# Performance work log

Measured on AMD Instinct MI355X. Metric: run time of the kernel, lower is better.

The kernel has to match this reference:

```python
import jax, jax.numpy as jnp
import numpy as np

NUM_HEADS = 16


def setup_inputs() -> dict:
    key = jax.random.key(0)
    k0, k1, k2, k3 = jax.random.split(key, 4)
    B, N, C = 8, 1024, 1024
    D = C // NUM_HEADS
    x = jax.random.normal(k0, (B, N, C), dtype=jnp.float32)
    # RoPE angle table [1, N, 1, head_dim]
    rope_freqs = jax.random.uniform(k1, (1, N, 1, D), dtype=jnp.float32) * (2.0 * jnp.pi)
    # qkv: Linear(dim, 3*dim, bias=False); proj: Linear(dim, dim) with bias
    qkv_w = jax.random.normal(k2, (3 * C, C), dtype=jnp.float32) * 0.02
    proj_w = jax.random.normal(k3, (C, C), dtype=jnp.float32) * 0.02
    proj_b = jnp.zeros((C,), dtype=jnp.float32)
    return {"x": x, "rope_freqs": rope_freqs, "qkv_w": qkv_w, "proj_w": proj_w, "proj_b": proj_b}


def _rotate_half(t):
    t1, t2 = jnp.split(t, 2, axis=-1)
    return jnp.concatenate([-t2, t1], axis=-1)


def reference(x, rope_freqs, qkv_w, proj_w, proj_b):
    B, N, C = x.shape
    H = NUM_HEADS
    D = C // H
    scale = D ** (-0.5)
    # QKV projection -> [3, B, H, N, D]
    qkv = (x @ qkv_w.T).reshape(B, N, 3, H, D).transpose(2, 0, 3, 1, 4)
    q, k, v = qkv[0], qkv[1], qkv[2]
    # RoPE: freqs [1, N, 1, D] -> [1, 1, N, D], applied to all tokens (n_special = 0)
    freqs = jnp.transpose(rope_freqs, (0, 2, 1, 3))
    cos = jnp.cos(freqs).astype(q.dtype)
    sin = jnp.sin(freqs).astype(q.dtype)
    q = q * cos + _rotate_half(q) * sin
    k = k * cos + _rotate_half(k) * sin
    # Full materialized attention (as in source)
    attn = jax.nn.softmax(jnp.einsum("bhnd,bhmd->bhnm", q, k) * scale, axis=-1)
    out = jnp.einsum("bhnm,bhmd->bhnd", attn, v)  # [B, H, N, D]
    out = out.transpose(0, 2, 1, 3).reshape(B, N, C)
    return out @ proj_w.T + proj_b
```

## Files before the change

### kernel.cpp

```cpp
#include <hip/hip_runtime.h>


typedef __attribute__((ext_vector_type(8))) short bf16x8;
typedef __attribute__((ext_vector_type(4))) float floatx4;
typedef __attribute__((ext_vector_type(4))) unsigned int u32x4;
typedef __attribute__((ext_vector_type(2))) unsigned int u32x2;

__device__ __forceinline__ void gld16(const void* g, void* l) {
  __builtin_amdgcn_global_load_lds((const __attribute__((address_space(1))) void*)g,
                                   (__attribute__((address_space(3))) void*)l, 16, 0, 0);
}

__device__ __forceinline__ short f2bf(float f) {
  unsigned u = __builtin_bit_cast(unsigned, f);
  u = (u + 0x7FFFu + ((u >> 16) & 1u)) >> 16;
  return (short)u;
}
__device__ __forceinline__ unsigned cvtpk(float lo, float hi) {
  unsigned r;
  asm("v_cvt_pk_bf16_f32 %0, %1, %2" : "=v"(r) : "v"(lo), "v"(hi));
  return r;
}
__device__ __forceinline__ float pexp(float x) {
  float r;
  asm("v_exp_f32 %0, %1" : "=v"(r) : "v"(x));
  return r;
}

__global__ __launch_bounds__(256) void prep_all(const float* __restrict__ sx,
                                                const float* __restrict__ sq,
                                                const float* __restrict__ sp,
                                                short* __restrict__ dst,
                                                const float* __restrict__ ropef,
                                                float2* __restrict__ tbl) {
  int bid = blockIdx.x;
  if (bid < 2048) {
    for (int i = bid * 256 + threadIdx.x; i < 3145728; i += 2048 * 256) {
      const float4* src;
      if (i < 2097152)      src = reinterpret_cast<const float4*>(sx) + i;
      else if (i < 2883584) src = reinterpret_cast<const float4*>(sq) + (i - 2097152);
      else                  src = reinterpret_cast<const float4*>(sp) + (i - 2883584);
      float4 v = *src;
      uint2 o;
      o.x = cvtpk(v.x, v.y);
      o.y = cvtpk(v.z, v.w);
      reinterpret_cast<uint2*>(dst)[i] = o;
    }
  } else {
    int i = (bid - 2048) * 256 + threadIdx.x;
    float v = ropef[i];
    tbl[i] = make_float2(cosf(v), sinf(v));
  }
}

#define QSCALE 0.18033688011112042f

__device__ __forceinline__ void gemm_main(const short* __restrict__ A,
                                          const short* __restrict__ Bm,
                                          short* As, short* Bs,
                                          floatx4 (&acc)[2][4],
                                          int bx, int by) {
  const int tid = threadIdx.x;
  const int wid = tid >> 6, lane = tid & 63;
  const int g = lane >> 4, l15 = lane & 15;
  const int wr = wid >> 2, wc = wid & 3;
  const size_t trow = (size_t)by * 128, tcol = (size_t)bx * 256;
  floatx4 zero = {0.f, 0.f, 0.f, 0.f};
  #pragma unroll
  for (int i = 0; i < 2; ++i)
    #pragma unroll
    for (int j = 0; j < 4; ++j) acc[i][j] = zero;

  auto stage = [&](int buf, int k0) {
    {
      const int cb = wid * 64;
      const int c  = cb + lane;
      const int r  = c >> 3, s = c & 7;
      const int koff = k0 + ((s ^ (r & 7)) << 3);
      gld16(A + (trow + r) * 1024 + koff, As + buf * 8192 + (size_t)cb * 8);
    }
    #pragma unroll
    for (int i = 0; i < 2; ++i) {
      const int cb = (i * 16 + wid) * 64;
      const int c  = cb + lane;
      const int r  = c >> 3, s = c & 7;
      const int koff = k0 + ((s ^ (r & 7)) << 3);
      gld16(Bm + (tcol + r) * 1024 + koff, Bs + buf * 16384 + (size_t)cb * 8);
    }
  };

  stage(0, 0);
  __syncthreads();

  for (int t = 0; t < 16; ++t) {
    const int buf = t & 1;
    if (t < 15) stage(buf ^ 1, (t + 1) * 64);
    const short* Ab = As + buf * 8192;
    const short* Bb = Bs + buf * 16384;
    #pragma unroll
    for (int ks = 0; ks < 2; ++ks) {
      bf16x8 af[2], bfr[4];
      #pragma unroll
      for (int mi = 0; mi < 2; ++mi) {
        int row = wr * 32 + mi * 16 + l15;
        int ch  = (ks * 4 + g) ^ (row & 7);
        af[mi] = *reinterpret_cast<const bf16x8*>(Ab + row * 64 + ch * 8);
      }
      #pragma unroll
      for (int nt = 0; nt < 4; ++nt) {
        int row = wc * 64 + nt * 16 + l15;
        int ch  = (ks * 4 + g) ^ (row & 7);
        bfr[nt] = *reinterpret_cast<const bf16x8*>(Bb + row * 64 + ch * 8);
      }
      __builtin_amdgcn_s_setprio(1);
      #pragma unroll
      for (int mi = 0; mi < 2; ++mi)
        #pragma unroll
        for (int nt = 0; nt < 4; ++nt)
          acc[mi][nt] = __builtin_amdgcn_mfma_f32_16x16x32_bf16(af[mi], bfr[nt],
                                                                acc[mi][nt], 0, 0, 0);
      __builtin_amdgcn_s_setprio(0);
    }
    __syncthreads();
  }
}

__global__ __launch_bounds__(1024, 4) void gemm_qkv_k(const short* __restrict__ A,
                                                      const short* __restrict__ Bm,
                                                      const float2* __restrict__ tbl,
                                                      short* __restrict__ qo,
                                                      short* __restrict__ ko,
                                                      short* __restrict__ vt) {
  extern __shared__ __align__(16) short smem[];
  short* As = smem;
  short* Bs = smem + 16384;
  const int id  = blockIdx.y * 12 + blockIdx.x;
  const int sid = (id & 7) * 96 + (id >> 3);
  const int bx  = sid % 12, by = sid / 12;
  floatx4 acc[2][4];
  gemm_main(A, Bm, As, Bs, acc, bx, by);

  const int tid = threadIdx.x;
  const int wid = tid >> 6, lane = tid & 63;
  const int g = lane >> 4, l15 = lane & 15;
  const int wr = wid >> 2, wc = wid & 3;
  const int trow = by * 128, tcol = bx * 256;
  const int which = bx >> 2;

  if (which < 2) {
    short* dst = which == 0 ? qo : ko;
    const float sc = which == 0 ? QSCALE : 1.0f;
    #pragma unroll
    for (int nt = 0; nt < 2; ++nt) {
      int col = tcol + wc * 64 + nt * 16 + l15;
      int hc = col & 1023, h = hc >> 6, d1 = hc & 63;
      #pragma unroll
      for (int mi = 0; mi < 2; ++mi)
        #pragma unroll
        for (int r = 0; r < 4; ++r) {
          int rowg = trow + wr * 32 + mi * 16 + g * 4 + r;
          int b = rowg >> 10, n = rowg & 1023;
          float a1 = acc[mi][nt][r], a2 = acc[mi][nt + 2][r];
          float2 c1 = tbl[n * 64 + d1];
          float2 c2 = tbl[n * 64 + d1 + 32];
          float o1 = (a1 * c1.x - a2 * c1.y) * sc;
          float o2 = (a2 * c2.x + a1 * c2.y) * sc;
          size_t base = ((size_t)(b * 16 + h) * 1024 + n) * 64;
          dst[base + d1]      = f2bf(o1);
          dst[base + d1 + 32] = f2bf(o2);
        }
    }
  } else {
    #pragma unroll
    for (int nt = 0; nt < 4; ++nt) {
      int col = tcol + wc * 64 + nt * 16 + l15;
      int hc = col & 1023, h = hc >> 6, d = hc & 63;
      #pragma unroll
      for (int mi = 0; mi < 2; ++mi) {
        int rowg = trow + wr * 32 + mi * 16 + g * 4;
        int b = rowg >> 10, n0 = rowg & 1023;
        ushort4 pk;
        pk.x = (unsigned short)f2bf(acc[mi][nt][0]);
        pk.y = (unsigned short)f2bf(acc[mi][nt][1]);
        pk.z = (unsigned short)f2bf(acc[mi][nt][2]);
        pk.w = (unsigned short)f2bf(acc[mi][nt][3]);
        *reinterpret_cast<ushort4*>((unsigned short*)vt +
            ((size_t)(b * 16 + h) * 64 + d) * 1024 + n0) = pk;
      }
    }
  }
}

__global__ __launch_bounds__(1024, 4) void gemm_proj_k(const short* __restrict__ A,
                                                       const short* __restrict__ Bm,
                                                       const float* __restrict__ pb,
                                                       float* __restrict__ out) {
  extern __shared__ __align__(16) short smem[];
  short* As = smem;
  short* Bs = smem + 16384;
  const int id  = blockIdx.y * 4 + blockIdx.x;
  const int sid = (id & 7) * 32 + (id >> 3);
  const int bx  = sid % 4, by = sid / 4;
  floatx4 acc[2][4];
  gemm_main(A, Bm, As, Bs, acc, bx, by);

  const int tid = threadIdx.x;
  const int wid = tid >> 6, lane = tid & 63;
  const int g = lane >> 4, l15 = lane & 15;
  const int wr = wid >> 2, wc = wid & 3;
  const int trow = by * 128, tcol = bx * 256;
  #pragma unroll
  for (int nt = 0; nt < 4; ++nt) {
    int col = tcol + wc * 64 + nt * 16 + l15;
    float bias = pb[col];
    #pragma unroll
    for (int mi = 0; mi < 2; ++mi)
      #pragma unroll
      for (int r = 0; r < 4; ++r) {
        int rowg = trow + wr * 32 + mi * 16 + g * 4 + r;
        out[(size_t)rowg * 1024 + col] = acc[mi][nt][r] + bias;
      }
  }
}

__global__ __launch_bounds__(256) void attn_kernel(const short* __restrict__ qs,
                                                   const short* __restrict__ ksrc,
                                                   const short* __restrict__ vt,
                                                   short* __restrict__ aout) {
  __shared__ __align__(16) short Kl[3][64 * 64];
  __shared__ __align__(16) short Vl[3][64 * 64];

  const int tid = threadIdx.x, wid = tid >> 6, lane = tid & 63;
  const int g = lane >> 4, l15 = lane & 15;
  const int bh = blockIdx.x, q0 = blockIdx.y * 256;
  const size_t bhoff = (size_t)bh * 1024 * 64;
  const short* Kb = ksrc + bhoff;
  const short* Vb = vt + bhoff;
  const int slb = (lane & 48) + ((lane >> 4) << 2);

  const short* QpA = qs + bhoff + (size_t)(q0 + wid * 16 + l15) * 64 + g * 8;
  bf16x8 qA0 = *reinterpret_cast<const bf16x8*>(QpA);
  bf16x8 qA1 = *reinterpret_cast<const bf16x8*>(QpA + 32);
  bf16x8 qB0 = *reinterpret_cast<const bf16x8*>(QpA + 64 * 64);
  bf16x8 qB1 = *reinterpret_cast<const bf16x8*>(QpA + 64 * 64 + 32);
  bf16x8 qC0 = *reinterpret_cast<const bf16x8*>(QpA + 128 * 64);
  bf16x8 qC1 = *reinterpret_cast<const bf16x8*>(QpA + 128 * 64 + 32);
  bf16x8 qD0 = *reinterpret_cast<const bf16x8*>(QpA + 192 * 64);
  bf16x8 qD1 = *reinterpret_cast<const bf16x8*>(QpA + 192 * 64 + 32);

  floatx4 oA[4], oB[4], oC[4], oD[4];
  floatx4 zero = {0.f, 0.f, 0.f, 0.f};
  #pragma unroll
  for (int i = 0; i < 4; ++i) { oA[i] = zero; oB[i] = zero; oC[i] = zero; oD[i] = zero; }
  float lrunA = 0.f, lrunB = 0.f, lrunC = 0.f, lrunD = 0.f;

  auto stage = [&](int buf, int t) {
    #pragma unroll
    for (int i = 0; i < 2; ++i) {
      const int cb = (i * 4 + wid) * 64;
      const int c = cb + lane;
      const int r = c >> 3, s = c & 7;
      const int off = (s ^ (r & 7)) << 3;
      gld16(Kb + (size_t)(t * 64 + r) * 64 + off, &Kl[buf][cb * 8]);
      gld16(Vb + (size_t)r * 1024 + t * 64 + off, &Vl[buf][cb * 8]);
    }
  };

#define SOFTSLICE(s_, lrun, pa)                                                \
  do {                                                                         \
    float p0 = pexp(s_[0][0]), p1 = pexp(s_[0][1]);                            \
    float p2 = pexp(s_[0][2]), p3 = pexp(s_[0][3]);                            \
    float p4 = pexp(s_[1][0]), p5 = pexp(s_[1][1]);                            \
    float p6 = pexp(s_[1][2]), p7 = pexp(s_[1][3]);                            \
    lrun += ((p0 + p1) + (p2 + p3)) + ((p4 + p5) + (p6 + p7));                 \
    unsigned wa0 = cvtpk(p0, p1), wa1 = cvtpk(p2, p3);                         \
    unsigned wb0 = cvtpk(p4, p5), wb1 = cvtpk(p6, p7);                         \
    u32x2 y0 = __builtin_amdgcn_permlane32_swap(wa0, wb0, false, false);       \
    u32x2 z0 = __builtin_amdgcn_permlane16_swap(y0[0], y0[1], false, false);   \
    u32x2 y1 = __builtin_amdgcn_permlane32_swap(wa1, wb1, false, false);       \
    u32x2 z1 = __builtin_amdgcn_permlane16_swap(y1[0], y1[1], false, false);   \
    u32x4 aw = {z0[0], z1[0], z0[1], z1[1]};                                   \
    pa = __builtin_bit_cast(bf16x8, aw);                                       \
  } while (0)

#define QKSLICE(base, sA_, sB_, sC_, sD_)                                      \
  __builtin_amdgcn_s_setprio(1);                                               \
  _Pragma("unroll")                                                            \
  for (int kk = 0; kk < 2; ++kk) {                                             \
    int krow = (base + kk) * 16 + l15;                                         \
    int ch0 = (g ^ (krow & 7)) << 3, ch1 = ((4 + g) ^ (krow & 7)) << 3;        \
    bf16x8 kf0 = *reinterpret_cast<const bf16x8*>(&Kl[btop][krow * 64 + ch0]); \
    sA_[kk] = __builtin_amdgcn_mfma_f32_16x16x32_bf16(kf0, qA0, sA_[kk],0,0,0);\
    sB_[kk] = __builtin_amdgcn_mfma_f32_16x16x32_bf16(kf0, qB0, sB_[kk],0,0,0);\
    sC_[kk] = __builtin_amdgcn_mfma_f32_16x16x32_bf16(kf0, qC0, sC_[kk],0,0,0);\
    sD_[kk] = __builtin_amdgcn_mfma_f32_16x16x32_bf16(kf0, qD0, sD_[kk],0,0,0);\
    bf16x8 kf1 = *reinterpret_cast<const bf16x8*>(&Kl[btop][krow * 64 + ch1]); \
    sA_[kk] = __builtin_amdgcn_mfma_f32_16x16x32_bf16(kf1, qA1, sA_[kk],0,0,0);\
    sB_[kk] = __builtin_amdgcn_mfma_f32_16x16x32_bf16(kf1, qB1, sB_[kk],0,0,0);\
    sC_[kk] = __builtin_amdgcn_mfma_f32_16x16x32_bf16(kf1, qC1, sC_[kk],0,0,0);\
    sD_[kk] = __builtin_amdgcn_mfma_f32_16x16x32_bf16(kf1, qD1, sD_[kk],0,0,0);\
  }                                                                            \
  __builtin_amdgcn_s_setprio(0);

#define PVSLICE(chsel, paA_, paB_, paC_, paD_)                                 \
  __builtin_amdgcn_s_setprio(1);                                               \
  _Pragma("unroll")                                                            \
  for (int nt = 0; nt < 4; ++nt) {                                             \
    int row = nt * 16 + l15;                                                   \
    int ch = (((chsel) + g) ^ (row & 7)) << 3;                                 \
    bf16x8 vf = *reinterpret_cast<const bf16x8*>(&Vl[btop][row * 64 + ch]);    \
    oA[nt] = __builtin_amdgcn_mfma_f32_16x16x32_bf16(paA_, vf, oA[nt],0,0,0);  \
    oB[nt] = __builtin_amdgcn_mfma_f32_16x16x32_bf16(paB_, vf, oB[nt],0,0,0);  \
    oC[nt] = __builtin_amdgcn_mfma_f32_16x16x32_bf16(paC_, vf, oC[nt],0,0,0);  \
    oD[nt] = __builtin_amdgcn_mfma_f32_16x16x32_bf16(paD_, vf, oD[nt],0,0,0);  \
  }                                                                            \
  __builtin_amdgcn_s_setprio(0);

  stage(0, 0);
  stage(1, 1);
  asm volatile("s_waitcnt vmcnt(4)" ::: "memory");
  __builtin_amdgcn_s_barrier();
  asm volatile("" ::: "memory");

  int btop = 0;
  for (int t = 0; t < 16; ++t) {
    if (t < 14) {
      int bnx = btop + 2; if (bnx >= 3) bnx -= 3;
      stage(bnx, t + 2);
    }

    {
      floatx4 sA[2], sB[2], sC[2], sD[2];
      #pragma unroll
      for (int kk = 0; kk < 2; ++kk) { sA[kk]=zero; sB[kk]=zero; sC[kk]=zero; sD[kk]=zero; }
      QKSLICE(0, sA, sB, sC, sD);
      bf16x8 paA, paB, paC, paD;
      SOFTSLICE(sA, lrunA, paA);
      SOFTSLICE(sB, lrunB, paB);
      SOFTSLICE(sC, lrunC, paC);
      SOFTSLICE(sD, lrunD, paD);
      PVSLICE(0, paA, paB, paC, paD);
    }
    {
      floatx4 sA[2], sB[2], sC[2], sD[2];
      #pragma unroll
      for (int kk = 0; kk < 2; ++kk) { sA[kk]=zero; sB[kk]=zero; sC[kk]=zero; sD[kk]=zero; }
      QKSLICE(2, sA, sB, sC, sD);
      bf16x8 paA, paB, paC, paD;
      SOFTSLICE(sA, lrunA, paA);
      SOFTSLICE(sB, lrunB, paB);
      SOFTSLICE(sC, lrunC, paC);
      SOFTSLICE(sD, lrunD, paD);
      PVSLICE(4, paA, paB, paC, paD);
    }

    if (t < 15) {
      if (t < 14) asm volatile("s_waitcnt vmcnt(4)" ::: "memory");
      else        asm volatile("s_waitcnt vmcnt(0)" ::: "memory");
      __builtin_amdgcn_s_barrier();
      asm volatile("" ::: "memory");
    }
    btop = btop + 1 == 3 ? 0 : btop + 1;
  }

  const int b = bh >> 4, h = bh & 15;
  lrunA += __shfl_xor(lrunA, 16); lrunA += __shfl_xor(lrunA, 32);
  lrunB += __shfl_xor(lrunB, 16); lrunB += __shfl_xor(lrunB, 32);
  lrunC += __shfl_xor(lrunC, 16); lrunC += __shfl_xor(lrunC, 32);
  lrunD += __shfl_xor(lrunD, 16); lrunD += __shfl_xor(lrunD, 32);
  float invA = 1.f / lrunA, invB = 1.f / lrunB;
  float invC = 1.f / lrunC, invD = 1.f / lrunD;
  #pragma unroll
  for (int r = 0; r < 4; ++r) {
    float irA = __shfl(invA, slb + r);
    float irB = __shfl(invB, slb + r);
    float irC = __shfl(invC, slb + r);
    float irD = __shfl(invD, slb + r);
    int nA = q0 + wid * 16 + g * 4 + r;
    size_t baseA = ((size_t)(b * 1024) + nA) * 1024 + h * 64;
    size_t baseB = baseA + (size_t)64 * 1024;
    size_t baseC = baseA + (size_t)128 * 1024;
    size_t baseD = baseA + (size_t)192 * 1024;
    #pragma unroll
    for (int nt = 0; nt < 4; ++nt) {
      aout[baseA + nt * 16 + l15] = f2bf(oA[nt][r] * irA);
      aout[baseB + nt * 16 + l15] = f2bf(oB[nt][r] * irB);
      aout[baseC + nt * 16 + l15] = f2bf(oC[nt][r] * irC);
      aout[baseD + nt * 16 + l15] = f2bf(oD[nt][r] * irD);
    }
  }
#undef SOFTSLICE
#undef QKSLICE
#undef PVSLICE
}

extern "C" void kernel_launch(void* const* d_in, const int* in_sizes, int n_in,
                              void* d_out, int out_size, void* d_ws, size_t ws_size,
                              hipStream_t stream) {
  const float* x      = (const float*)d_in[0];
  const float* ropef  = (const float*)d_in[1];
  const float* qkv_w  = (const float*)d_in[2];
  const float* proj_w = (const float*)d_in[3];
  const float* proj_b = (const float*)d_in[4];
  float* out = (float*)d_out;

  char* ws = (char*)d_ws;
  short*  xb  = (short*)(ws + 0);
  short*  wqb = (short*)(ws + 16777216);
  short*  wpb = (short*)(ws + 23068672);
  short*  qb  = (short*)(ws + 25165824);
  short*  kb  = (short*)(ws + 41943040);
  short*  vtb = (short*)(ws + 58720256);
  short*  aob = (short*)(ws + 75497472);
  float2* tbl = (float2*)(ws + 92274688);

  prep_all<<<2304, 256, 0, stream>>>(x, qkv_w, proj_w, xb, ropef, tbl);

  gemm_qkv_k<<<dim3(12, 64), 1024, 98304, stream>>>(xb, wqb, tbl, qb, kb, vtb);
  attn_kernel<<<dim3(128, 4), 256, 0, stream>>>(qb, kb, vtb, aob);
  gemm_proj_k<<<dim3(4, 64), 1024, 98304, stream>>>(aob, wpb, proj_b, out);
}
```

Before: 155.7 us.

## Fuse x fp32-to-bf16 conversion into QKV GEMM A-tile staging

The separate pass that converted x to bf16 in the prep kernel is removed. The QKV GEMM now loads fp32 A tiles into registers, converts them with cvt_pk, and writes them to LDS after the MFMA work on the current buffer. This drops a 32MB read plus 16MB write round trip. In exchange, the GEMM reads twice the A bytes from global memory through registers rather than async global_load_lds, which adds register pressure and exposes more load latency.

```diff
diff --git a/kernel.cpp b/kernel.cpp
--- a/kernel.cpp
+++ b/kernel.cpp
@@ -27,27 +27,24 @@
   return r;
 }
 
-__global__ __launch_bounds__(256) void prep_all(const float* __restrict__ sx,
-                                                const float* __restrict__ sq,
+__global__ __launch_bounds__(256) void prep_all(const float* __restrict__ sq,
                                                 const float* __restrict__ sp,
                                                 short* __restrict__ dst,
                                                 const float* __restrict__ ropef,
                                                 float2* __restrict__ tbl) {
   int bid = blockIdx.x;
-  if (bid < 2048) {
-    for (int i = bid * 256 + threadIdx.x; i < 3145728; i += 2048 * 256) {
-      const float4* src;
-      if (i < 2097152)      src = reinterpret_cast<const float4*>(sx) + i;
-      else if (i < 2883584) src = reinterpret_cast<const float4*>(sq) + (i - 2097152);
-      else                  src = reinterpret_cast<const float4*>(sp) + (i - 2883584);
-      float4 v = *src;
-      uint2 o;
-      o.x = cvtpk(v.x, v.y);
-      o.y = cvtpk(v.z, v.w);
-      reinterpret_cast<uint2*>(dst)[i] = o;
-    }
+  if (bid < 4096) {
+    int i = bid * 256 + threadIdx.x;
+    const float4* src;
+    if (i < 786432) src = reinterpret_cast<const float4*>(sq) + i;
+    else            src = reinterpret_cast<const float4*>(sp) + (i - 786432);
+    float4 v = *src;
+    uint2 o;
+    o.x = cvtpk(v.x, v.y);
+    o.y = cvtpk(v.z, v.w);
+    reinterpret_cast<uint2*>(dst)[i] = o;
   } else {
-    int i = (bid - 2048) * 256 + threadIdx.x;
+    int i = (bid - 4096) * 256 + threadIdx.x;
     float v = ropef[i];
     tbl[i] = make_float2(cosf(v), sinf(v));
   }
@@ -55,7 +52,9 @@
 
 #define QSCALE 0.18033688011112042f
 
-__device__ __forceinline__ void gemm_main(const short* __restrict__ A,
+template <bool AF32>
+__device__ __forceinline__ void gemm_main(const float* __restrict__ Af,
+                                          const short* __restrict__ Ab16,
                                           const short* __restrict__ Bm,
                                           short* As, short* Bs,
                                           floatx4 (&acc)[2][4],
@@ -71,30 +70,54 @@
     #pragma unroll
     for (int j = 0; j < 4; ++j) acc[i][j] = zero;
 
-  auto stage = [&](int buf, int k0) {
-    {
-      const int cb = wid * 64;
-      const int c  = cb + lane;
-      const int r  = c >> 3, s = c & 7;
-      const int koff = k0 + ((s ^ (r & 7)) << 3);
-      gld16(A + (trow + r) * 1024 + koff, As + buf * 8192 + (size_t)cb * 8);
-    }
+  const int rA = tid >> 3, sA = tid & 7;
+  const int swzA = (sA ^ (rA & 7)) << 3;
+
+  auto stageB = [&](int buf, int k0) {
     #pragma unroll
     for (int i = 0; i < 2; ++i) {
       const int cb = (i * 16 + wid) * 64;
       const int c  = cb + lane;
       const int r  = c >> 3, s = c & 7;
       const int koff = k0 + ((s ^ (r & 7)) << 3);
-      gld16(Bm + (tcol + r) * 1024 + koff, Bs + buf * 16384 + (size_t)cb * 8);
+      gld16(Bm + (tcol + r) * 1024 + koff, Bs + buf * 16384 + (size_t)c * 8);
     }
   };
-
-  stage(0, 0);
+  auto stageA16 = [&](int buf, int k0) {
+    const int koff = k0 + swzA;
+    gld16(Ab16 + (trow + rA) * 1024 + koff, As + buf * 8192 + (size_t)tid * 8);
+  };
+
+  float4 fa0, fa1;
+  auto aload = [&](int k0) {
+    const float* p = Af + (trow + rA) * 1024 + k0 + swzA;
+    fa0 = *reinterpret_cast<const float4*>(p);
+    fa1 = *reinterpret_cast<const float4*>(p + 4);
+  };
+  auto awrite = [&](int buf) {
+    u32x4 w = {cvtpk(fa0.x, fa0.y), cvtpk(fa0.z, fa0.w),
+               cvtpk(fa1.x, fa1.y), cvtpk(fa1.z, fa1.w)};
+    *reinterpret_cast<bf16x8*>(As + buf * 8192 + (size_t)tid * 8) =
+        __builtin_bit_cast(bf16x8, w);
+  };
+
+  if constexpr (AF32) {
+    aload(0);
+    stageB(0, 0);
+    awrite(0);
+  } else {
+    stageA16(0, 0);
+    stageB(0, 0);
+  }
   __syncthreads();
 
   for (int t = 0; t < 16; ++t) {
     const int buf = t & 1;
-    if (t < 15) stage(buf ^ 1, (t + 1) * 64);
+    if (t < 15) {
+      if constexpr (AF32) aload((t + 1) * 64);
+      else                stageA16(buf ^ 1, (t + 1) * 64);
+      stageB(buf ^ 1, (t + 1) * 64);
+    }
     const short* Ab = As + buf * 8192;
     const short* Bb = Bs + buf * 16384;
     #pragma unroll
@@ -121,11 +144,14 @@
                                                                 acc[mi][nt], 0, 0, 0);
       __builtin_amdgcn_s_setprio(0);
     }
+    if (t < 15) {
+      if constexpr (AF32) awrite(buf ^ 1);
+    }
     __syncthreads();
   }
 }
 
-__global__ __launch_bounds__(1024, 4) void gemm_qkv_k(const short* __restrict__ A,
+__global__ __launch_bounds__(1024, 4) void gemm_qkv_k(const float* __restrict__ Af,
                                                       const short* __restrict__ Bm,
                                                       const float2* __restrict__ tbl,
                                                       short* __restrict__ qo,
@@ -138,7 +164,7 @@
   const int sid = (id & 7) * 96 + (id >> 3);
   const int bx  = sid % 12, by = sid / 12;
   floatx4 acc[2][4];
-  gemm_main(A, Bm, As, Bs, acc, bx, by);
+  gemm_main<true>(Af, nullptr, Bm, As, Bs, acc, bx, by);
 
   const int tid = threadIdx.x;
   const int wid = tid >> 6, lane = tid & 63;
@@ -202,7 +228,7 @@
   const int sid = (id & 7) * 32 + (id >> 3);
   const int bx  = sid % 4, by = sid / 4;
   floatx4 acc[2][4];
-  gemm_main(A, Bm, As, Bs, acc, bx, by);
+  gemm_main<false>(nullptr, A, Bm, As, Bs, acc, bx, by);
 
   const int tid = threadIdx.x;
   const int wid = tid >> 6, lane = tid & 63;
@@ -405,7 +431,6 @@
   float* out = (float*)d_out;
 
   char* ws = (char*)d_ws;
-  short*  xb  = (short*)(ws + 0);
   short*  wqb = (short*)(ws + 16777216);
   short*  wpb = (short*)(ws + 23068672);
   short*  qb  = (short*)(ws + 25165824);
@@ -414,9 +439,9 @@
   short*  aob = (short*)(ws + 75497472);
   float2* tbl = (float2*)(ws + 92274688);
 
-  prep_all<<<2304, 256, 0, stream>>>(x, qkv_w, proj_w, xb, ropef, tbl);
-
-  gemm_qkv_k<<<dim3(12, 64), 1024, 98304, stream>>>(xb, wqb, tbl, qb, kb, vtb);
+  prep_all<<<4352, 256, 0, stream>>>(qkv_w, proj_w, wqb, ropef, tbl);
+
+  gemm_qkv_k<<<dim3(12, 64), 1024, 98304, stream>>>(x, wqb, tbl, qb, kb, vtb);
   attn_kernel<<<dim3(128, 4), 256, 0, stream>>>(qb, kb, vtb, aob);
   gemm_proj_k<<<dim3(4, 64), 1024, 98304, stream>>>(aob, wpb, proj_b, out);
 }
```

Result: no change. 158.4 us (+1.7%).
